# Performance work log

Hardware: AMD Instinct MI355X
Metric: run time of the kernel (lower is better)

Reference implementation:

```python
import jax, jax.numpy as jnp
import numpy as np

H = W = 240

def setup_inputs() -> dict:
    key = jax.random.key(0)
    k1, k2, k3 = jax.random.split(key, 3)
    B = 256
    T2_Gen = jax.random.normal(k1, (B, 1, H, W), dtype=jnp.float32)
    underT2_K = jax.random.normal(k2, (B, 2, H, W), dtype=jnp.float32)
    # k-space sampling mask (soft in [0,1); original uses a fixed undersampling mask)
    A = jax.random.uniform(k3, (H, W), dtype=jnp.float32)
    return {"T2_Gen": T2_Gen, "underT2_K": underT2_K, "A": A}

def reference(T2_Gen, underT2_K, A):
    # x2: [B, H, W]
    x2 = T2_Gen.reshape(-1, H, W)
    # batched 2D FFT over the last two axes (replaces the per-slice numpy loop)
    x2_k = jnp.fft.fft2(x2)  # complex64
    # undersampled k-space as complex: real = channel 0, imag = channel 1
    y_k = underT2_K[:, 0, :, :] + 1j * underT2_K[:, 1, :, :]
    z_k = (1.0 - A) * x2_k + y_k
    z = jnp.abs(jnp.fft.ifft2(z_k))  # [B, H, W] real
    return z.reshape(-1, 1, H, W)
```

## Files before the change

kernel.cpp:

```cpp
#include <hip/hip_runtime.h>
#include <hip/hip_fp16.h>
#include <math.h>

#define HW 240
#define PITCH 242
#define SMF_PITCH (2*PITCH)
#define IMG_PIX (HW*HW)
#define NB 15
#define TILE_ELEMS (240*16)

__device__ __forceinline__ float2 cmul(float2 a, float2 b){
    return make_float2(a.x*b.x - a.y*b.y, a.x*b.y + a.y*b.x);
}
__device__ __forceinline__ float2 cadd(float2 a, float2 b){
    return make_float2(a.x+b.x, a.y+b.y);
}
__device__ __forceinline__ float2 csub(float2 a, float2 b){
    return make_float2(a.x-b.x, a.y-b.y);
}
__device__ __forceinline__ __half2 f2h(float2 a){ return __floats2half2_rn(a.x, a.y); }
__device__ __forceinline__ float2 h2f(__half2 h){ return make_float2(__low2float(h), __high2float(h)); }

__device__ __forceinline__ void wave_fence(){ __builtin_amdgcn_wave_barrier(); }

template<int SIGN>
__device__ __forceinline__ void dft15(const float2* x, float2* X){
    const float S = (float)SIGN;
    const float s3 = 0.8660254037844387f;
    float2 y[5][3];
    #pragma unroll
    for (int n2 = 0; n2 < 5; ++n2){
        float2 a0 = x[n2], a1 = x[5+n2], a2 = x[10+n2];
        float2 t = cadd(a1, a2);
        float2 u = csub(a1, a2);
        float2 m = make_float2(a0.x - 0.5f*t.x, a0.y - 0.5f*t.y);
        float sx = S * s3;
        float2 s = make_float2(-sx*u.y, sx*u.x);
        y[n2][0] = cadd(a0, t);
        y[n2][1] = cadd(m, s);
        y[n2][2] = csub(m, s);
    }
    const float C15[9] = {1.f, 0.9135454576426009f, 0.6691306063588582f, 0.30901699437494745f,
                          -0.10452846326765346f, -0.5f, -0.8090169943749475f,
                          -0.9781476007338057f, -0.9781476007338057f};
    const float S15[9] = {0.f, 0.4067366430758004f, 0.7431448254773942f, 0.9510565162951535f,
                          0.9945218953682733f, 0.8660254037844387f, 0.5877852522924731f,
                          0.20791169081775931f, -0.20791169081775931f};
    #pragma unroll
    for (int n2 = 1; n2 < 5; ++n2){
        #pragma unroll
        for (int k1 = 1; k1 < 3; ++k1){
            const int e = n2*k1;
            y[n2][k1] = cmul(y[n2][k1], make_float2(C15[e], S*S15[e]));
        }
    }
    const float c1 = 0.30901699437494745f, s1 = 0.9510565162951535f;
    const float c2 = -0.8090169943749475f, s2 = 0.5877852522924731f;
    #pragma unroll
    for (int k1 = 0; k1 < 3; ++k1){
        float2 x0 = y[0][k1], x1 = y[1][k1], x2 = y[2][k1], x3 = y[3][k1], x4 = y[4][k1];
        float2 t1 = cadd(x1, x4), t3 = csub(x1, x4);
        float2 t2 = cadd(x2, x3), t4 = csub(x2, x3);
        X[k1] = make_float2(x0.x + t1.x + t2.x, x0.y + t1.y + t2.y);
        float2 u1 = make_float2(x0.x + c1*t1.x + c2*t2.x, x0.y + c1*t1.y + c2*t2.y);
        float2 u2 = make_float2(x0.x + c2*t1.x + c1*t2.x, x0.y + c2*t1.y + c1*t2.y);
        float2 v1 = make_float2(S*(s1*t3.x + s2*t4.x), S*(s1*t3.y + s2*t4.y));
        float2 v2 = make_float2(S*(s2*t3.x - s1*t4.x), S*(s2*t3.y - s1*t4.y));
        X[k1+3]  = make_float2(u1.x - v1.y, u1.y + v1.x);
        X[k1+12] = make_float2(u1.x + v1.y, u1.y - v1.x);
        X[k1+6]  = make_float2(u2.x - v2.y, u2.y + v2.x);
        X[k1+9]  = make_float2(u2.x + v2.y, u2.y - v2.x);
    }
}

template<int SIGN>
__device__ __forceinline__ void dft16(const float2* x, float2* X){
    const float S = (float)SIGN;
    float2 y[4][4];
    #pragma unroll
    for (int n2 = 0; n2 < 4; ++n2){
        float2 a0 = x[n2], a1 = x[4+n2], a2 = x[8+n2], a3 = x[12+n2];
        float2 t0 = cadd(a0,a2), t1 = csub(a0,a2);
        float2 t2 = cadd(a1,a3), t3 = csub(a1,a3);
        float2 it3 = make_float2(-S*t3.y, S*t3.x);
        y[n2][0] = cadd(t0,t2);
        y[n2][2] = csub(t0,t2);
        y[n2][1] = cadd(t1,it3);
        y[n2][3] = csub(t1,it3);
    }
    const float C16[10] = {1.f, 0.9238795325112867f, 0.7071067811865476f, 0.3826834323650898f,
                           0.f, -0.3826834323650898f, -0.7071067811865476f, -0.9238795325112867f,
                           -1.f, -0.9238795325112867f};
    const float S16[10] = {0.f, 0.3826834323650898f, 0.7071067811865476f, 0.9238795325112867f,
                           1.f, 0.9238795325112867f, 0.7071067811865476f, 0.3826834323650898f,
                           0.f, -0.3826834323650898f};
    #pragma unroll
    for (int n2 = 1; n2 < 4; ++n2){
        #pragma unroll
        for (int k1 = 1; k1 < 4; ++k1){
            const int e = n2*k1;
            y[n2][k1] = cmul(y[n2][k1], make_float2(C16[e], S*S16[e]));
        }
    }
    #pragma unroll
    for (int k1 = 0; k1 < 4; ++k1){
        float2 a0 = y[0][k1], a1 = y[1][k1], a2 = y[2][k1], a3 = y[3][k1];
        float2 t0 = cadd(a0,a2), t1 = csub(a0,a2);
        float2 t2 = cadd(a1,a3), t3 = csub(a1,a3);
        float2 it3 = make_float2(-S*t3.y, S*t3.x);
        X[k1]    = cadd(t0,t2);
        X[k1+8]  = csub(t0,t2);
        X[k1+4]  = cadd(t1,it3);
        X[k1+12] = csub(t1,it3);
    }
}

template<int SIGN>
__device__ void fft240(float2 (*sm)[PITCH], float2* v, int rl, int b){
    const float TWOPI = 6.28318530717958647692f;
    float2 Y[15];
    dft15<SIGN>(v, Y);
    float2 step, tw = make_float2(1.0f, 0.0f);
    {
        float ang = (float)SIGN * TWOPI * (float)b * (1.0f/240.0f);
        __sincosf(ang, &step.y, &step.x);
    }
    #pragma unroll
    for (int d = 0; d < 15; ++d){
        sm[rl][b*15 + d] = cmul(Y[d], tw);
        tw = cmul(tw, step);
    }
    wave_fence();
    float2 Z[16];
    if (b < 15){
        #pragma unroll
        for (int bb = 0; bb < 16; ++bb) Z[bb] = sm[rl][bb*15 + b];
    }
    wave_fence();
    if (b < 15){
        float2 XX[16];
        dft16<SIGN>(Z, XX);
        #pragma unroll
        for (int m = 0; m < 16; ++m) sm[rl][15*m + b] = XX[m];
    }
    wave_fence();
}

__global__ __launch_bounds__(256) void passA_rowfft(const float* __restrict__ x,
                                                    __half2* __restrict__ out){
    __shared__ __align__(16) float2 sm[16][PITCH];
    float* smf = (float*)sm;
    int g = blockIdx.x, img = g / NB, h0 = (g % NB) * 16;
    int tid = threadIdx.x, rl = tid >> 4, b = tid & 15;
    const float* src = x + (size_t)img * IMG_PIX + (size_t)h0 * HW;
    if (tid < 240){
        #pragma unroll
        for (int jj = 0; jj < 4; ++jj){
            int k = jj*240 + tid;
            int r = k / 60, c = 4*(k - r*60);
            float4 d = *(const float4*)(src + 4*k);
            *(float4*)(smf + r*SMF_PITCH + c) = d;
        }
    }
    __syncthreads();
    float2 v[15];
    #pragma unroll
    for (int a = 0; a < 15; ++a) v[a] = make_float2(smf[rl*SMF_PITCH + 16*a + b], 0.0f);
    wave_fence();
    fft240<-1>(sm, v, rl, b);
    #pragma unroll
    for (int kb = 0; kb < NB; ++kb){
        float2 val = sm[rl][kb*16 + b];
        out[((size_t)(img*NB + kb)*HW + h0 + rl)*16 + b] = f2h(val);
    }
}

__global__ __launch_bounds__(256) void passB_col_dc_icol(__half2* __restrict__ io,
                                                         const float* __restrict__ under,
                                                         const float* __restrict__ Am){
    __shared__ __align__(16) float2 sm[16][PITCH];
    int g = blockIdx.x, img = g / NB, s = g % NB, kw0 = s * 16;
    int tid = threadIdx.x, rl = tid >> 4, b = tid & 15;
    __half2* chunk = io + (size_t)(img*NB + s) * TILE_ELEMS;
    if (tid < 240){
        #pragma unroll
        for (int jj = 0; jj < 4; ++jj){
            int k = jj*240 + tid;
            float4 raw = *(const float4*)(chunk + 4*k);
            const __half2* hp = (const __half2*)&raw;
            int col = k >> 2;
            int r0 = (4*k) & 15;
            #pragma unroll
            for (int i = 0; i < 4; ++i) sm[r0 + i][col] = h2f(hp[i]);
        }
    }
    __syncthreads();
    float2 v[15];
    #pragma unroll
    for (int a = 0; a < 15; ++a) v[a] = sm[rl][16*a + b];
    wave_fence();
    fft240<-1>(sm, v, rl, b);
    __syncthreads();

    const float* y0 = under + (size_t)img * (2*IMG_PIX);
    const float* y1 = y0 + IMG_PIX;
    #pragma unroll
    for (int j = 0; j < 15; ++j){
        int kh = j*16 + rl;
        size_t p = (size_t)kh * HW + kw0 + b;
        float sc = 1.0f - Am[p];
        float2 X = sm[b][kh];
        sm[b][kh] = make_float2(sc * X.x + y0[p], sc * X.y + y1[p]);
    }
    __syncthreads();
    #pragma unroll
    for (int a = 0; a < 15; ++a) v[a] = sm[rl][16*a + b];
    wave_fence();
    fft240<+1>(sm, v, rl, b);
    __syncthreads();

    const float inv240 = 1.0f / 240.0f;
    if (tid < 240){
        #pragma unroll
        for (int jj = 0; jj < 4; ++jj){
            int k = jj*240 + tid;
            int col = k >> 2;
            int r0 = (4*k) & 15;
            float4 outv;
            __half2* op = (__half2*)&outv;
            #pragma unroll
            for (int i = 0; i < 4; ++i){
                float2 val = sm[r0 + i][col];
                op[i] = f2h(make_float2(val.x*inv240, val.y*inv240));
            }
            *(float4*)(chunk + 4*k) = outv;
        }
    }
}

__global__ __launch_bounds__(256) void passC_irow_abs(const __half2* __restrict__ in,
                                                      float* __restrict__ outp){
    __shared__ __align__(16) float2 sm[16][PITCH];
    int g = blockIdx.x, img = g / NB, h0 = (g % NB) * 16;
    int tid = threadIdx.x, rl = tid >> 4, b = tid & 15;
    #pragma unroll
    for (int kb = 0; kb < NB; ++kb){
        __half2 hv = in[((size_t)(img*NB + kb)*HW + h0 + rl)*16 + b];
        sm[rl][kb*16 + b] = h2f(hv);
    }
    wave_fence();
    float2 v[15];
    #pragma unroll
    for (int a = 0; a < 15; ++a) v[a] = sm[rl][16*a + b];
    wave_fence();
    fft240<+1>(sm, v, rl, b);
    __syncthreads();
    float* dst = outp + (size_t)img * IMG_PIX + (size_t)h0 * HW;
    const float inv240 = 1.0f / 240.0f;
    if (tid < 240){
        #pragma unroll
        for (int jj = 0; jj < 4; ++jj){
            int k = jj*240 + tid;
            int r = k / 60, c = 4*(k - r*60);
            float4 o;
            float2 X0 = sm[r][c+0], X1 = sm[r][c+1], X2 = sm[r][c+2], X3 = sm[r][c+3];
            o.x = sqrtf(X0.x*X0.x + X0.y*X0.y) * inv240;
            o.y = sqrtf(X1.x*X1.x + X1.y*X1.y) * inv240;
            o.z = sqrtf(X2.x*X2.x + X2.y*X2.y) * inv240;
            o.w = sqrtf(X3.x*X3.x + X3.y*X3.y) * inv240;
            *(float4*)(dst + 4*k) = o;
        }
    }
}

extern "C" void kernel_launch(void* const* d_in, const int* in_sizes, int n_in,
                              void* d_out, int out_size, void* d_ws, size_t ws_size,
                              hipStream_t stream){
    const float* T2   = (const float*)d_in[0];
    const float* U    = (const float*)d_in[1];
    const float* Am   = (const float*)d_in[2];
    float* out        = (float*)d_out;

    const int B = 256;
    __half2* i1 = (__half2*)d_ws;

    dim3 grid(B * NB), block(256);
    passA_rowfft     <<<grid, block, 0, stream>>>(T2, i1);
    passB_col_dc_icol<<<grid, block, 0, stream>>>(i1, U, Am);
    passC_irow_abs   <<<grid, block, 0, stream>>>(i1, out);
}
```

Before: 274.2 us.

## Pack two real rows per complex FFT in row pass and prefetch k-space data

The row FFT pass now packs two real input rows into the real and imaginary parts of one complex 240-point FFT. It then separates the two spectra using conjugate symmetry, so each block handles 30 rows and the grid shrinks to 8 blocks per image. This halves the row-FFT arithmetic and the number of blocks. The column pass also issues the undersampled k-space loads into registers before the FFT, hiding their latency behind compute at the cost of more live registers.

```diff
diff --git a/kernel.cpp b/kernel.cpp
--- a/kernel.cpp
+++ b/kernel.cpp
@@ -4,9 +4,10 @@
 
 #define HW 240
 #define PITCH 242
-#define SMF_PITCH (2*PITCH)
 #define IMG_PIX (HW*HW)
 #define NB 15
+#define NBA 8
+#define AF_PITCH 244
 #define TILE_ELEMS (240*16)
 
 __device__ __forceinline__ float2 cmul(float2 a, float2 b){
@@ -148,30 +149,46 @@
 
 __global__ __launch_bounds__(256) void passA_rowfft(const float* __restrict__ x,
                                                     __half2* __restrict__ out){
-    __shared__ __align__(16) float2 sm[16][PITCH];
-    float* smf = (float*)sm;
-    int g = blockIdx.x, img = g / NB, h0 = (g % NB) * 16;
+    __shared__ __align__(16) float smraw[30*AF_PITCH];
+    float2 (*sm)[PITCH] = (float2(*)[PITCH])smraw;
+    int g = blockIdx.x, img = g / NBA, h0 = (g % NBA) * 30;
     int tid = threadIdx.x, rl = tid >> 4, b = tid & 15;
     const float* src = x + (size_t)img * IMG_PIX + (size_t)h0 * HW;
-    if (tid < 240){
-        #pragma unroll
-        for (int jj = 0; jj < 4; ++jj){
-            int k = jj*240 + tid;
-            int r = k / 60, c = 4*(k - r*60);
-            float4 d = *(const float4*)(src + 4*k);
-            *(float4*)(smf + r*SMF_PITCH + c) = d;
-        }
-    }
-    __syncthreads();
-    float2 v[15];
-    #pragma unroll
-    for (int a = 0; a < 15; ++a) v[a] = make_float2(smf[rl*SMF_PITCH + 16*a + b], 0.0f);
-    wave_fence();
-    fft240<-1>(sm, v, rl, b);
-    #pragma unroll
-    for (int kb = 0; kb < NB; ++kb){
-        float2 val = sm[rl][kb*16 + b];
-        out[((size_t)(img*NB + kb)*HW + h0 + rl)*16 + b] = f2h(val);
+    #pragma unroll
+    for (int j = 0; j < 7; ++j){
+        int f = j*256 + tid;
+        int r = f / 60, c4 = f - r*60;
+        float4 d = *(const float4*)(src + 4*f);
+        *(float4*)(smraw + r*AF_PITCH + 4*c4) = d;
+    }
+    if (tid < 8){
+        int f = 1792 + tid;
+        int r = f / 60, c4 = f - r*60;
+        float4 d = *(const float4*)(src + 4*f);
+        *(float4*)(smraw + r*AF_PITCH + 4*c4) = d;
+    }
+    __syncthreads();
+    if (tid < 240){
+        float2 v[15];
+        #pragma unroll
+        for (int a = 0; a < 15; ++a)
+            v[a] = make_float2(smraw[(2*rl)*AF_PITCH + 16*a + b],
+                               smraw[(2*rl+1)*AF_PITCH + 16*a + b]);
+        __syncthreads();
+        fft240<-1>(sm, v, rl, b);
+        #pragma unroll
+        for (int kb = 0; kb < NB; ++kb){
+            int k = kb*16 + b;
+            int km = k ? 240 - k : 0;
+            float2 P = sm[rl][k], Q = sm[rl][km];
+            float2 Xa = make_float2(0.5f*(P.x + Q.x), 0.5f*(P.y - Q.y));
+            float2 Xb = make_float2(0.5f*(P.y + Q.y), 0.5f*(Q.x - P.x));
+            size_t o = ((size_t)(img*NB + kb)*HW + (h0 + 2*rl))*16 + b;
+            out[o]      = f2h(Xa);
+            out[o + 16] = f2h(Xb);
+        }
+    } else {
+        __syncthreads();
     }
 }
 
@@ -182,12 +199,30 @@
     int g = blockIdx.x, img = g / NB, s = g % NB, kw0 = s * 16;
     int tid = threadIdx.x, rl = tid >> 4, b = tid & 15;
     __half2* chunk = io + (size_t)(img*NB + s) * TILE_ELEMS;
+
+    float4 raw[4];
     if (tid < 240){
         #pragma unroll
         for (int jj = 0; jj < 4; ++jj){
             int k = jj*240 + tid;
-            float4 raw = *(const float4*)(chunk + 4*k);
-            const __half2* hp = (const __half2*)&raw;
+            raw[jj] = *(const float4*)(chunk + 4*k);
+        }
+    }
+    const float* y0 = under + (size_t)img * (2*IMG_PIX);
+    const float* y1 = y0 + IMG_PIX;
+    float y0r[15], y1r[15];
+    #pragma unroll
+    for (int j = 0; j < 15; ++j){
+        size_t p = (size_t)(j*16 + rl) * HW + kw0 + b;
+        y0r[j] = y0[p];
+        y1r[j] = y1[p];
+    }
+
+    if (tid < 240){
+        #pragma unroll
+        for (int jj = 0; jj < 4; ++jj){
+            int k = jj*240 + tid;
+            const __half2* hp = (const __half2*)&raw[jj];
             int col = k >> 2;
             int r0 = (4*k) & 15;
             #pragma unroll
@@ -202,15 +237,13 @@
     fft240<-1>(sm, v, rl, b);
     __syncthreads();
 
-    const float* y0 = under + (size_t)img * (2*IMG_PIX);
-    const float* y1 = y0 + IMG_PIX;
     #pragma unroll
     for (int j = 0; j < 15; ++j){
         int kh = j*16 + rl;
         size_t p = (size_t)kh * HW + kw0 + b;
         float sc = 1.0f - Am[p];
         float2 X = sm[b][kh];
-        sm[b][kh] = make_float2(sc * X.x + y0[p], sc * X.y + y1[p]);
+        sm[b][kh] = make_float2(sc * X.x + y0r[j], sc * X.y + y1r[j]);
     }
     __syncthreads();
     #pragma unroll
@@ -284,8 +317,8 @@
     const int B = 256;
     __half2* i1 = (__half2*)d_ws;
 
-    dim3 grid(B * NB), block(256);
-    passA_rowfft     <<<grid, block, 0, stream>>>(T2, i1);
-    passB_col_dc_icol<<<grid, block, 0, stream>>>(i1, U, Am);
-    passC_irow_abs   <<<grid, block, 0, stream>>>(i1, out);
-}
+    dim3 block(256);
+    passA_rowfft     <<<dim3(B * NBA), block, 0, stream>>>(T2, i1);
+    passB_col_dc_icol<<<dim3(B * NB),  block, 0, stream>>>(i1, U, Am);
+    passC_irow_abs   <<<dim3(B * NB),  block, 0, stream>>>(i1, U != nullptr ? out : out);
+}
```

Measured after the change: 281.0 us. +2.5%, slower.
